# Performance work log

Measured on AMD Instinct MI355X. Metric: run time of the kernel, lower is better.

The kernel has to match this reference:

```python
import jax, jax.numpy as jnp
import numpy as np

B = 65536      # batch
HID = 128      # hidden_dim
Q = 4          # IRK stages
DT = 0.1       # default time step
N_ITERS = 10   # fixed-point iterations


def setup_inputs() -> dict:
    key = jax.random.key(0)
    ks = jax.random.split(key, 16)
    def lin(k, fan_in, fan_out):
        return jax.random.normal(k, (fan_in, fan_out), jnp.float32) / np.sqrt(fan_in)
    return {
        "X0": jax.random.normal(ks[0], (B, 4), jnp.float32),
        "W1": lin(ks[1], 4, HID),   "b1": jnp.zeros((HID,), jnp.float32),
        "W2": lin(ks[2], HID, HID), "b2": jnp.zeros((HID,), jnp.float32),
        "W3": lin(ks[3], HID, HID), "b3": jnp.zeros((HID,), jnp.float32),
        "W4": lin(ks[4], HID, 4),   "b4": jnp.zeros((4,), jnp.float32),
        "lam1": jax.random.normal(ks[5], (1,), jnp.float32) * 0.1 + 0.5,
        "lam2": jax.random.normal(ks[6], (1,), jnp.float32) * 0.1 + 0.5,
        "lam3": jax.random.normal(ks[7], (1,), jnp.float32) * 0.1 + 0.5,
        "lam4": jax.random.normal(ks[8], (1,), jnp.float32) * 0.1 + 0.5,
        "IRK_alpha": jax.random.normal(ks[9], (Q, Q), jnp.float32) * 0.25,
        "IRK_beta": jax.random.normal(ks[10], (Q,), jnp.float32) * 0.25,
    }


def reference(X0, W1, b1, W2, b2, W3, b3, W4, b4,
              lam1, lam2, lam3, lam4, IRK_alpha, IRK_beta):
    dt = DT

    def mlp(x):  # (N,4) -> (N,4)
        h = jnp.tanh(x @ W1 + b1)
        h = jnp.tanh(h @ W2 + b2)
        h = jnp.tanh(h @ W3 + b3)
        return h @ W4 + b4

    def hamiltonian_vf(x):  # x: (N,4) = [p1,p2,q1,q2]
        H_out = mlp(x)
        dp_dt = -lam1 * H_out[:, 2:] - lam2 * x[:, 2:]
        dq_dt = lam3 * H_out[:, :2] + lam4 * x[:, :2]
        return jnp.concatenate([dp_dt, dq_dt], axis=1)

    bsz = X0.shape[0]
    K = jnp.zeros((bsz, Q, 4), X0.dtype)
    for _ in range(N_ITERS):  # small fixed trip count, unrolled
        # same contraction as original torch einsum 'bqi,ij->bqj'
        X_stages = X0[:, None, :] + dt * jnp.einsum('bqi,ij->bqj', K, IRK_alpha)
        K = hamiltonian_vf(X_stages.reshape(-1, 4)).reshape(bsz, Q, 4)

    # intended IRK final combine: X1 = X0 + dt * sum_q beta_q K[:,q,:]
    X1 = X0 + dt * jnp.einsum('bqi,q->bi', K, IRK_beta)
    return X1
```

## Files before the change

kernel.cpp:

```cpp
#include <hip/hip_runtime.h>
#include <hip/hip_bf16.h>
#include <stdint.h>

#define HID    128
#define DT     0.1f
#define NITER  10
#define NTHR   512
#define NW     8
#define RPW    32
#define NBLK   256
#define NCH    4
#define SCALE  2.885390081777927f

typedef __attribute__((ext_vector_type(8))) short bf16x8;
typedef __attribute__((ext_vector_type(4))) float f32x4;
typedef __attribute__((ext_vector_type(2))) unsigned int u32x2;
typedef __attribute__((ext_vector_type(4))) unsigned int u32x4;

union FragU { bf16x8 v; uint32_t u[4]; };

struct alignas(16) Smem {
    uint32_t w2f[8 * 4 * 64 * 4];
    uint32_t w3f[8 * 4 * 64 * 4];
    uint32_t w1f[8 * 64 * 4];
    float    b1[HID], b2[HID], b3[HID];
    uint16_t hbuf[NW * RPW * HID];
};

__device__ __forceinline__ uint16_t f2bf(float f) {
    uint32_t u = __float_as_uint(f);
    return (uint16_t)((u + 0x7fffu + ((u >> 16) & 1u)) >> 16);
}

__device__ __forceinline__ uint32_t pk2(float a, float b) {
    __hip_bfloat162 h = __float22bfloat162_rn(float2{a, b});
    return *reinterpret_cast<uint32_t*>(&h);
}

__device__ __forceinline__ float tanh_pre(float y) {
    float e = __builtin_amdgcn_exp2f(y);
    return fmaf(-2.0f, __builtin_amdgcn_rcpf(e + 1.0f), 1.0f);
}

__device__ __forceinline__ float uread(const float* p) {
    return __uint_as_float(__builtin_amdgcn_readfirstlane(__float_as_uint(*p)));
}

__device__ __forceinline__ void hstore(char* hb, int row, int ot, int g, const f32x4& a) {
    int off = row * 256 + ((32 * ot + 8 * g) ^ ((row & 7) << 4));
    u32x2 p;
    p.x = pk2(tanh_pre(a[0]), tanh_pre(a[1]));
    p.y = pk2(tanh_pre(a[2]), tanh_pre(a[3]));
    *(u32x2*)(hb + off) = p;
}

__device__ __forceinline__ bf16x8 hload(const char* hb, int row, int kt, int g) {
    int off = row * 256 + ((64 * kt + 16 * g) ^ ((row & 7) << 4));
    return *(const bf16x8*)(hb + off);
}

__device__ __forceinline__ void dense_layer(
    char* hb, const uint32_t* __restrict__ wf, const float* __restrict__ bias,
    int ln, int g, int lane)
{
    bf16x8 hf[2][4];
    #pragma unroll
    for (int ct = 0; ct < 2; ++ct)
        #pragma unroll
        for (int kt = 0; kt < 4; ++kt)
            hf[ct][kt] = hload(hb, ct * 16 + ln, kt, g);
    #pragma unroll
    for (int ot = 0; ot < 8; ++ot) {
        f32x4 bs = *(const f32x4*)&bias[ot * 16 + 4 * g];
        f32x4 aA = bs, aB = bs;
        #pragma unroll
        for (int kt = 0; kt < 4; ++kt) {
            bf16x8 wfr = *(const bf16x8*)&wf[((ot * 4 + kt) * 64 + lane) * 4];
            aA = __builtin_amdgcn_mfma_f32_16x16x32_bf16(wfr, hf[0][kt], aA, 0, 0, 0);
            aB = __builtin_amdgcn_mfma_f32_16x16x32_bf16(wfr, hf[1][kt], aB, 0, 0, 0);
        }
        hstore(hb, ln, ot, g, aA);
        hstore(hb, 16 + ln, ot, g, aB);
    }
}

__global__ __launch_bounds__(NTHR, 2) void pinn_irk_rows(
    const float* __restrict__ x0g,
    const float* __restrict__ w1g, const float* __restrict__ b1g,
    const float* __restrict__ w2g, const float* __restrict__ b2g,
    const float* __restrict__ w3g, const float* __restrict__ b3g,
    const float* __restrict__ w4g, const float* __restrict__ b4g,
    const float* __restrict__ l1g, const float* __restrict__ l2g,
    const float* __restrict__ l3g, const float* __restrict__ l4g,
    const float* __restrict__ alg, const float* __restrict__ beg,
    float* __restrict__ outg)
{
    __shared__ Smem S;
    const int t    = threadIdx.x;
    const int blk  = blockIdx.x;
    const int lane = t & 63;
    const int w    = t >> 6;
    const int ln   = lane & 15;
    const int g    = lane >> 4;
    const bool owner = (g == 0);

    const float L0 = uread(l1g), L1v = uread(l2g), L2v = uread(l3g), L3v = uread(l4g);
    const float B40 = uread(b4g), B41 = uread(b4g + 1);
    const float B42 = uread(b4g + 2), B43 = uread(b4g + 3);
    const float BE0 = uread(beg), BE1 = uread(beg + 1);
    const float BE2 = uread(beg + 2), BE3 = uread(beg + 3);
    float A[16];
    #pragma unroll
    for (int i = 0; i < 16; ++i) A[i] = uread(alg + i);

    for (int s = t; s < 2048; s += NTHR) {
        int lane_s = s & 63, kto = s >> 6;
        int kt = kto & 3, ot = kto >> 2;
        int m = ot * 16 + (lane_s & 15), gs = lane_s >> 4;
        uint32_t f2[4], f3[4];
        #pragma unroll
        for (int jj = 0; jj < 4; ++jj) {
            int k = kt * 32 + 8 * gs + 2 * jj;
            f2[jj] = (uint32_t)f2bf(w2g[k * HID + m] * SCALE)
                   | ((uint32_t)f2bf(w2g[(k + 1) * HID + m] * SCALE) << 16);
            f3[jj] = (uint32_t)f2bf(w3g[k * HID + m] * SCALE)
                   | ((uint32_t)f2bf(w3g[(k + 1) * HID + m] * SCALE) << 16);
        }
        *(u32x4*)&S.w2f[s * 4] = (u32x4){f2[0], f2[1], f2[2], f2[3]};
        *(u32x4*)&S.w3f[s * 4] = (u32x4){f3[0], f3[1], f3[2], f3[3]};
    }
    {
        int lane_s = t & 63, ot = t >> 6;
        int gs = lane_s >> 4;
        uint32_t f[4] = {0u, 0u, 0u, 0u};
        if (gs == 0) {
            int m = ot * 16 + (lane_s & 15);
            f[0] = (uint32_t)f2bf(w1g[0 * HID + m] * SCALE)
                 | ((uint32_t)f2bf(w1g[1 * HID + m] * SCALE) << 16);
            f[1] = (uint32_t)f2bf(w1g[2 * HID + m] * SCALE)
                 | ((uint32_t)f2bf(w1g[3 * HID + m] * SCALE) << 16);
        }
        *(u32x4*)&S.w1f[t * 4] = (u32x4){f[0], f[1], f[2], f[3]};
    }
    if (t < HID) {
        S.b1[t] = b1g[t] * SCALE;
        S.b2[t] = b2g[t] * SCALE;
        S.b3[t] = b3g[t] * SCALE;
    }
    bf16x8 w4f[4];
    #pragma unroll
    for (int kt = 0; kt < 4; ++kt) {
        bf16x8 f;
        #pragma unroll
        for (int j = 0; j < 8; ++j) {
            int k = kt * 32 + 8 * g + j;
            f[j] = (ln < 4) ? (short)f2bf(w4g[k * 4 + ln]) : (short)0;
        }
        w4f[kt] = f;
    }
    __syncthreads();

    char* hb = (char*)&S.hbuf[w * RPW * HID];

    for (int ch = 0; ch < NCH; ++ch) {
        const int base = ((blk * NW + w) * NCH + ch) * RPW;
        f32x4 XA0 = *(const f32x4*)&x0g[((base + ln) >> 2) * 4];
        f32x4 XB0 = *(const f32x4*)&x0g[((base + 16 + ln) >> 2) * 4];
        f32x4 XA = XA0, XB = XB0;
        f32x4 kvA = {0.f,0.f,0.f,0.f}, kvB = {0.f,0.f,0.f,0.f};

        #pragma unroll 1
        for (int it = 0; it < NITER; ++it) {
            FragU xa, xb;
            xa.u[0] = owner ? pk2(XA[0], XA[1]) : 0u;
            xa.u[1] = owner ? pk2(XA[2], XA[3]) : 0u;
            xa.u[2] = 0u; xa.u[3] = 0u;
            xb.u[0] = owner ? pk2(XB[0], XB[1]) : 0u;
            xb.u[1] = owner ? pk2(XB[2], XB[3]) : 0u;
            xb.u[2] = 0u; xb.u[3] = 0u;

            #pragma unroll
            for (int ot = 0; ot < 8; ++ot) {
                f32x4 bs = *(const f32x4*)&S.b1[ot * 16 + 4 * g];
                bf16x8 wfr = *(const bf16x8*)&S.w1f[(ot * 64 + lane) * 4];
                f32x4 aA = __builtin_amdgcn_mfma_f32_16x16x32_bf16(wfr, xa.v, bs, 0, 0, 0);
                f32x4 aB = __builtin_amdgcn_mfma_f32_16x16x32_bf16(wfr, xb.v, bs, 0, 0, 0);
                hstore(hb, ln, ot, g, aA);
                hstore(hb, 16 + ln, ot, g, aB);
            }
            dense_layer(hb, S.w2f, S.b2, ln, g, lane);
            dense_layer(hb, S.w3f, S.b3, ln, g, lane);

            {
                bf16x8 hf[2][4];
                #pragma unroll
                for (int ct = 0; ct < 2; ++ct)
                    #pragma unroll
                    for (int kt = 0; kt < 4; ++kt)
                        hf[ct][kt] = hload(hb, ct * 16 + ln, kt, g);
                f32x4 kA = {0.f,0.f,0.f,0.f}, kB = {0.f,0.f,0.f,0.f};
                #pragma unroll
                for (int kt = 0; kt < 4; ++kt) {
                    kA = __builtin_amdgcn_mfma_f32_16x16x32_bf16(w4f[kt], hf[0][kt], kA, 0, 0, 0);
                    kB = __builtin_amdgcn_mfma_f32_16x16x32_bf16(w4f[kt], hf[1][kt], kB, 0, 0, 0);
                }
                float h0 = kA[0] + B40, h1 = kA[1] + B41;
                float h2 = kA[2] + B42, h3 = kA[3] + B43;
                kvA = (f32x4){-L0 * h2 - L1v * XA[2], -L0 * h3 - L1v * XA[3],
                               L2v * h0 + L3v * XA[0],  L2v * h1 + L3v * XA[1]};
                h0 = kB[0] + B40; h1 = kB[1] + B41;
                h2 = kB[2] + B42; h3 = kB[3] + B43;
                kvB = (f32x4){-L0 * h2 - L1v * XB[2], -L0 * h3 - L1v * XB[3],
                               L2v * h0 + L3v * XB[0],  L2v * h1 + L3v * XB[1]};
                #pragma unroll
                for (int c = 0; c < 4; ++c) {
                    float sA = kvA[0] * A[c] + kvA[1] * A[4 + c]
                             + kvA[2] * A[8 + c] + kvA[3] * A[12 + c];
                    float sB = kvB[0] * A[c] + kvB[1] * A[4 + c]
                             + kvB[2] * A[8 + c] + kvB[3] * A[12 + c];
                    XA[c] = fmaf(DT, sA, XA0[c]);
                    XB[c] = fmaf(DT, sB, XB0[c]);
                }
            }
        }

        if (owner) {
            *(f32x4*)(hb + ln * 16)        = kvA;
            *(f32x4*)(hb + (16 + ln) * 16) = kvB;
        }
        if (lane < 32) {
            const float* kk = (const float*)hb;
            int bl_ = lane >> 2, i = lane & 3;
            float s = BE0 * kk[(bl_ * 4 + 0) * 4 + i]
                    + BE1 * kk[(bl_ * 4 + 1) * 4 + i]
                    + BE2 * kk[(bl_ * 4 + 2) * 4 + i]
                    + BE3 * kk[(bl_ * 4 + 3) * 4 + i];
            int idx = base + lane;
            outg[idx] = x0g[idx] + DT * s;
        }
    }
}

extern "C" void kernel_launch(void* const* d_in, const int* in_sizes, int n_in,
                              void* d_out, int out_size, void* d_ws, size_t ws_size,
                              hipStream_t stream) {
    (void)in_sizes; (void)n_in; (void)d_ws; (void)ws_size; (void)out_size;

    dim3 grid(NBLK);
    dim3 block(NTHR);

    pinn_irk_rows<<<grid, block, 0, stream>>>(
        (const float*)d_in[0],
        (const float*)d_in[1],  (const float*)d_in[2],
        (const float*)d_in[3],  (const float*)d_in[4],
        (const float*)d_in[5],  (const float*)d_in[6],
        (const float*)d_in[7],  (const float*)d_in[8],
        (const float*)d_in[9],  (const float*)d_in[10],
        (const float*)d_in[11], (const float*)d_in[12],
        (const float*)d_in[13], (const float*)d_in[14],
        (float*)d_out);
}
```

Baseline: 405.6 us.

## Split rows across twice as many waves and batch tanh reciprocals

Doubles the block to 1024 threads (16 waves), so each wave handles 16 rows per chunk instead of 32 and issues one MFMA chain instead of two interleaved ones. This is meant to raise occupancy and latency hiding per CU. The cost is that each row now pulls twice as much weight-fragment traffic from LDS, and each wave has less instruction-level parallelism. The tanh is rewritten to compute four values with a single clamped reciprocal plus extra multiplies, cutting transcendental ops at some rounding risk. The launch bound asks for 4 blocks per CU, which may force tight register limits and cause spills.

```diff
diff --git a/kernel.cpp b/kernel.cpp
--- a/kernel.cpp
+++ b/kernel.cpp
@@ -5,9 +5,9 @@
 #define HID    128
 #define DT     0.1f
 #define NITER  10
-#define NTHR   512
-#define NW     8
-#define RPW    32
+#define NTHR   1024
+#define NW     16
+#define RPW    16
 #define NBLK   256
 #define NCH    4
 #define SCALE  2.885390081777927f
@@ -37,9 +37,23 @@
     return *reinterpret_cast<uint32_t*>(&h);
 }
 
-__device__ __forceinline__ float tanh_pre(float y) {
-    float e = __builtin_amdgcn_exp2f(y);
-    return fmaf(-2.0f, __builtin_amdgcn_rcpf(e + 1.0f), 1.0f);
+__device__ __forceinline__ f32x4 tanh4(f32x4 y) {
+    float e0 = __builtin_amdgcn_exp2f(fminf(y[0], 30.f)) + 1.0f;
+    float e1 = __builtin_amdgcn_exp2f(fminf(y[1], 30.f)) + 1.0f;
+    float e2 = __builtin_amdgcn_exp2f(fminf(y[2], 30.f)) + 1.0f;
+    float e3 = __builtin_amdgcn_exp2f(fminf(y[3], 30.f)) + 1.0f;
+    float p01   = e0 * e1;
+    float p012  = p01 * e2;
+    float p0123 = p012 * e3;
+    float r     = __builtin_amdgcn_rcpf(p0123);
+    float i3   = p012 * r;
+    float r012 = e3 * r;
+    float i2   = p01 * r012;
+    float r01  = e2 * r012;
+    float i1   = e0 * r01;
+    float i0   = e1 * r01;
+    return (f32x4){fmaf(-2.f, i0, 1.f), fmaf(-2.f, i1, 1.f),
+                   fmaf(-2.f, i2, 1.f), fmaf(-2.f, i3, 1.f)};
 }
 
 __device__ __forceinline__ float uread(const float* p) {
@@ -47,10 +61,11 @@
 }
 
 __device__ __forceinline__ void hstore(char* hb, int row, int ot, int g, const f32x4& a) {
+    f32x4 tq = tanh4(a);
     int off = row * 256 + ((32 * ot + 8 * g) ^ ((row & 7) << 4));
     u32x2 p;
-    p.x = pk2(tanh_pre(a[0]), tanh_pre(a[1]));
-    p.y = pk2(tanh_pre(a[2]), tanh_pre(a[3]));
+    p.x = pk2(tq[0], tq[1]);
+    p.y = pk2(tq[2], tq[3]);
     *(u32x2*)(hb + off) = p;
 }
 
@@ -63,28 +78,23 @@
     char* hb, const uint32_t* __restrict__ wf, const float* __restrict__ bias,
     int ln, int g, int lane)
 {
-    bf16x8 hf[2][4];
-    #pragma unroll
-    for (int ct = 0; ct < 2; ++ct)
-        #pragma unroll
-        for (int kt = 0; kt < 4; ++kt)
-            hf[ct][kt] = hload(hb, ct * 16 + ln, kt, g);
+    bf16x8 hf[4];
+    #pragma unroll
+    for (int kt = 0; kt < 4; ++kt)
+        hf[kt] = hload(hb, ln, kt, g);
     #pragma unroll
     for (int ot = 0; ot < 8; ++ot) {
-        f32x4 bs = *(const f32x4*)&bias[ot * 16 + 4 * g];
-        f32x4 aA = bs, aB = bs;
+        f32x4 a = *(const f32x4*)&bias[ot * 16 + 4 * g];
         #pragma unroll
         for (int kt = 0; kt < 4; ++kt) {
             bf16x8 wfr = *(const bf16x8*)&wf[((ot * 4 + kt) * 64 + lane) * 4];
-            aA = __builtin_amdgcn_mfma_f32_16x16x32_bf16(wfr, hf[0][kt], aA, 0, 0, 0);
-            aB = __builtin_amdgcn_mfma_f32_16x16x32_bf16(wfr, hf[1][kt], aB, 0, 0, 0);
-        }
-        hstore(hb, ln, ot, g, aA);
-        hstore(hb, 16 + ln, ot, g, aB);
-    }
-}
-
-__global__ __launch_bounds__(NTHR, 2) void pinn_irk_rows(
+            a = __builtin_amdgcn_mfma_f32_16x16x32_bf16(wfr, hf[kt], a, 0, 0, 0);
+        }
+        hstore(hb, ln, ot, g, a);
+    }
+}
+
+__global__ __launch_bounds__(NTHR, 4) void pinn_irk_rows(
     const float* __restrict__ x0g,
     const float* __restrict__ w1g, const float* __restrict__ b1g,
     const float* __restrict__ w2g, const float* __restrict__ b2g,
@@ -129,7 +139,7 @@
         *(u32x4*)&S.w2f[s * 4] = (u32x4){f2[0], f2[1], f2[2], f2[3]};
         *(u32x4*)&S.w3f[s * 4] = (u32x4){f3[0], f3[1], f3[2], f3[3]};
     }
-    {
+    if (t < 512) {
         int lane_s = t & 63, ot = t >> 6;
         int gs = lane_s >> 4;
         uint32_t f[4] = {0u, 0u, 0u, 0u};
@@ -165,70 +175,52 @@
     for (int ch = 0; ch < NCH; ++ch) {
         const int base = ((blk * NW + w) * NCH + ch) * RPW;
         f32x4 XA0 = *(const f32x4*)&x0g[((base + ln) >> 2) * 4];
-        f32x4 XB0 = *(const f32x4*)&x0g[((base + 16 + ln) >> 2) * 4];
-        f32x4 XA = XA0, XB = XB0;
-        f32x4 kvA = {0.f,0.f,0.f,0.f}, kvB = {0.f,0.f,0.f,0.f};
+        f32x4 XA = XA0;
+        f32x4 kvA = {0.f, 0.f, 0.f, 0.f};
 
         #pragma unroll 1
         for (int it = 0; it < NITER; ++it) {
-            FragU xa, xb;
+            FragU xa;
             xa.u[0] = owner ? pk2(XA[0], XA[1]) : 0u;
             xa.u[1] = owner ? pk2(XA[2], XA[3]) : 0u;
             xa.u[2] = 0u; xa.u[3] = 0u;
-            xb.u[0] = owner ? pk2(XB[0], XB[1]) : 0u;
-            xb.u[1] = owner ? pk2(XB[2], XB[3]) : 0u;
-            xb.u[2] = 0u; xb.u[3] = 0u;
 
             #pragma unroll
             for (int ot = 0; ot < 8; ++ot) {
                 f32x4 bs = *(const f32x4*)&S.b1[ot * 16 + 4 * g];
                 bf16x8 wfr = *(const bf16x8*)&S.w1f[(ot * 64 + lane) * 4];
-                f32x4 aA = __builtin_amdgcn_mfma_f32_16x16x32_bf16(wfr, xa.v, bs, 0, 0, 0);
-                f32x4 aB = __builtin_amdgcn_mfma_f32_16x16x32_bf16(wfr, xb.v, bs, 0, 0, 0);
-                hstore(hb, ln, ot, g, aA);
-                hstore(hb, 16 + ln, ot, g, aB);
+                f32x4 a = __builtin_amdgcn_mfma_f32_16x16x32_bf16(wfr, xa.v, bs, 0, 0, 0);
+                hstore(hb, ln, ot, g, a);
             }
             dense_layer(hb, S.w2f, S.b2, ln, g, lane);
             dense_layer(hb, S.w3f, S.b3, ln, g, lane);
 
             {
-                bf16x8 hf[2][4];
+                bf16x8 hf[4];
                 #pragma unroll
-                for (int ct = 0; ct < 2; ++ct)
-                    #pragma unroll
-                    for (int kt = 0; kt < 4; ++kt)
-                        hf[ct][kt] = hload(hb, ct * 16 + ln, kt, g);
-                f32x4 kA = {0.f,0.f,0.f,0.f}, kB = {0.f,0.f,0.f,0.f};
+                for (int kt = 0; kt < 4; ++kt)
+                    hf[kt] = hload(hb, ln, kt, g);
+                f32x4 kA = {0.f, 0.f, 0.f, 0.f};
                 #pragma unroll
-                for (int kt = 0; kt < 4; ++kt) {
-                    kA = __builtin_amdgcn_mfma_f32_16x16x32_bf16(w4f[kt], hf[0][kt], kA, 0, 0, 0);
-                    kB = __builtin_amdgcn_mfma_f32_16x16x32_bf16(w4f[kt], hf[1][kt], kB, 0, 0, 0);
-                }
+                for (int kt = 0; kt < 4; ++kt)
+                    kA = __builtin_amdgcn_mfma_f32_16x16x32_bf16(w4f[kt], hf[kt], kA, 0, 0, 0);
                 float h0 = kA[0] + B40, h1 = kA[1] + B41;
                 float h2 = kA[2] + B42, h3 = kA[3] + B43;
                 kvA = (f32x4){-L0 * h2 - L1v * XA[2], -L0 * h3 - L1v * XA[3],
                                L2v * h0 + L3v * XA[0],  L2v * h1 + L3v * XA[1]};
-                h0 = kB[0] + B40; h1 = kB[1] + B41;
-                h2 = kB[2] + B42; h3 = kB[3] + B43;
-                kvB = (f32x4){-L0 * h2 - L1v * XB[2], -L0 * h3 - L1v * XB[3],
-                               L2v * h0 + L3v * XB[0],  L2v * h1 + L3v * XB[1]};
                 #pragma unroll
                 for (int c = 0; c < 4; ++c) {
-                    float sA = kvA[0] * A[c] + kvA[1] * A[4 + c]
-                             + kvA[2] * A[8 + c] + kvA[3] * A[12 + c];
-                    float sB = kvB[0] * A[c] + kvB[1] * A[4 + c]
-                             + kvB[2] * A[8 + c] + kvB[3] * A[12 + c];
-                    XA[c] = fmaf(DT, sA, XA0[c]);
-                    XB[c] = fmaf(DT, sB, XB0[c]);
+                    float s = kvA[0] * A[c] + kvA[1] * A[4 + c]
+                            + kvA[2] * A[8 + c] + kvA[3] * A[12 + c];
+                    XA[c] = fmaf(DT, s, XA0[c]);
                 }
             }
         }
 
         if (owner) {
-            *(f32x4*)(hb + ln * 16)        = kvA;
-            *(f32x4*)(hb + (16 + ln) * 16) = kvB;
-        }
-        if (lane < 32) {
+            *(f32x4*)(hb + ln * 16) = kvA;
+        }
+        if (lane < 16) {
             const float* kk = (const float*)hb;
             int bl_ = lane >> 2, i = lane & 3;
             float s = BE0 * kk[(bl_ * 4 + 0) * 4 + i]
```

Result: slower. 474.8 us (+17.1%).

## Keep MLP activations in registers by permuting K ordering instead of LDS round-trips

Applied to the files above, without the earlier changes.

Each layer's MFMA output is now packed directly into the next layer's B-operand fragments in registers. The K index ordering of W1..W4 is permuted so the accumulator layout matches the fragment layout, which removes the per-layer LDS store and reload of the hidden activations. The LDS hidden buffer shrinks to a small K scratch area. The grid doubles and chunks per wave halve, and s_setprio is raised around the MFMA bursts. The cost is more live registers for the eight accumulator tiles per row group, which could pressure occupancy under the two-blocks-per-CU bound.

```diff
diff --git a/kernel.cpp b/kernel.cpp
--- a/kernel.cpp
+++ b/kernel.cpp
@@ -7,14 +7,12 @@
 #define NITER  10
 #define NTHR   512
 #define NW     8
-#define RPW    32
-#define NBLK   256
-#define NCH    4
+#define NBLK   512
+#define NCH    2
 #define SCALE  2.885390081777927f
 
 typedef __attribute__((ext_vector_type(8))) short bf16x8;
 typedef __attribute__((ext_vector_type(4))) float f32x4;
-typedef __attribute__((ext_vector_type(2))) unsigned int u32x2;
 typedef __attribute__((ext_vector_type(4))) unsigned int u32x4;
 
 union FragU { bf16x8 v; uint32_t u[4]; };
@@ -24,7 +22,7 @@
     uint32_t w3f[8 * 4 * 64 * 4];
     uint32_t w1f[8 * 64 * 4];
     float    b1[HID], b2[HID], b3[HID];
-    uint16_t hbuf[NW * RPW * HID];
+    float    kk[NW * 32 * 4];
 };
 
 __device__ __forceinline__ uint16_t f2bf(float f) {
@@ -46,45 +44,43 @@
     return __uint_as_float(__builtin_amdgcn_readfirstlane(__float_as_uint(*p)));
 }
 
-__device__ __forceinline__ void hstore(char* hb, int row, int ot, int g, const f32x4& a) {
-    int off = row * 256 + ((32 * ot + 8 * g) ^ ((row & 7) << 4));
-    u32x2 p;
-    p.x = pk2(tanh_pre(a[0]), tanh_pre(a[1]));
-    p.y = pk2(tanh_pre(a[2]), tanh_pre(a[3]));
-    *(u32x2*)(hb + off) = p;
-}
-
-__device__ __forceinline__ bf16x8 hload(const char* hb, int row, int kt, int g) {
-    int off = row * 256 + ((64 * kt + 16 * g) ^ ((row & 7) << 4));
-    return *(const bf16x8*)(hb + off);
-}
-
-__device__ __forceinline__ void dense_layer(
-    char* hb, const uint32_t* __restrict__ wf, const float* __restrict__ bias,
-    int ln, int g, int lane)
+__device__ __forceinline__ void packfr(const f32x4 (&a)[8], bf16x8 (&bfr)[4]) {
+    #pragma unroll
+    for (int kt = 0; kt < 4; ++kt) {
+        FragU f;
+        f.u[0] = pk2(tanh_pre(a[2 * kt][0]),     tanh_pre(a[2 * kt][1]));
+        f.u[1] = pk2(tanh_pre(a[2 * kt][2]),     tanh_pre(a[2 * kt][3]));
+        f.u[2] = pk2(tanh_pre(a[2 * kt + 1][0]), tanh_pre(a[2 * kt + 1][1]));
+        f.u[3] = pk2(tanh_pre(a[2 * kt + 1][2]), tanh_pre(a[2 * kt + 1][3]));
+        bfr[kt] = f.v;
+    }
+}
+
+__device__ __forceinline__ void dense_reg(
+    const uint32_t* __restrict__ wf, const float* __restrict__ bias,
+    bf16x8 (&bfrA)[4], bf16x8 (&bfrB)[4], int lane, int g)
 {
-    bf16x8 hf[2][4];
-    #pragma unroll
-    for (int ct = 0; ct < 2; ++ct)
-        #pragma unroll
-        for (int kt = 0; kt < 4; ++kt)
-            hf[ct][kt] = hload(hb, ct * 16 + ln, kt, g);
+    f32x4 aA[8], aB[8];
     #pragma unroll
     for (int ot = 0; ot < 8; ++ot) {
         f32x4 bs = *(const f32x4*)&bias[ot * 16 + 4 * g];
-        f32x4 aA = bs, aB = bs;
+        aA[ot] = bs; aB[ot] = bs;
+    }
+    __builtin_amdgcn_s_setprio(1);
+    #pragma unroll
+    for (int ot = 0; ot < 8; ++ot)
         #pragma unroll
         for (int kt = 0; kt < 4; ++kt) {
             bf16x8 wfr = *(const bf16x8*)&wf[((ot * 4 + kt) * 64 + lane) * 4];
-            aA = __builtin_amdgcn_mfma_f32_16x16x32_bf16(wfr, hf[0][kt], aA, 0, 0, 0);
-            aB = __builtin_amdgcn_mfma_f32_16x16x32_bf16(wfr, hf[1][kt], aB, 0, 0, 0);
-        }
-        hstore(hb, ln, ot, g, aA);
-        hstore(hb, 16 + ln, ot, g, aB);
-    }
-}
-
-__global__ __launch_bounds__(NTHR, 2) void pinn_irk_rows(
+            aA[ot] = __builtin_amdgcn_mfma_f32_16x16x32_bf16(wfr, bfrA[kt], aA[ot], 0, 0, 0);
+            aB[ot] = __builtin_amdgcn_mfma_f32_16x16x32_bf16(wfr, bfrB[kt], aB[ot], 0, 0, 0);
+        }
+    __builtin_amdgcn_s_setprio(0);
+    packfr(aA, bfrA);
+    packfr(aB, bfrB);
+}
+
+__global__ __launch_bounds__(NTHR, 2) void pinn_irk_reg(
     const float* __restrict__ x0g,
     const float* __restrict__ w1g, const float* __restrict__ b1g,
     const float* __restrict__ w2g, const float* __restrict__ b2g,
@@ -120,7 +116,7 @@
         uint32_t f2[4], f3[4];
         #pragma unroll
         for (int jj = 0; jj < 4; ++jj) {
-            int k = kt * 32 + 8 * gs + 2 * jj;
+            int k = 16 * (2 * kt + (jj >> 1)) + 4 * gs + 2 * (jj & 1);
             f2[jj] = (uint32_t)f2bf(w2g[k * HID + m] * SCALE)
                    | ((uint32_t)f2bf(w2g[(k + 1) * HID + m] * SCALE) << 16);
             f3[jj] = (uint32_t)f2bf(w3g[k * HID + m] * SCALE)
@@ -129,7 +125,7 @@
         *(u32x4*)&S.w2f[s * 4] = (u32x4){f2[0], f2[1], f2[2], f2[3]};
         *(u32x4*)&S.w3f[s * 4] = (u32x4){f3[0], f3[1], f3[2], f3[3]};
     }
-    {
+    if (t < 512) {
         int lane_s = t & 63, ot = t >> 6;
         int gs = lane_s >> 4;
         uint32_t f[4] = {0u, 0u, 0u, 0u};
@@ -153,21 +149,19 @@
         bf16x8 f;
         #pragma unroll
         for (int j = 0; j < 8; ++j) {
-            int k = kt * 32 + 8 * g + j;
+            int k = 16 * (2 * kt + (j >> 2)) + 4 * g + (j & 3);
             f[j] = (ln < 4) ? (short)f2bf(w4g[k * 4 + ln]) : (short)0;
         }
         w4f[kt] = f;
     }
     __syncthreads();
 
-    char* hb = (char*)&S.hbuf[w * RPW * HID];
-
     for (int ch = 0; ch < NCH; ++ch) {
-        const int base = ((blk * NW + w) * NCH + ch) * RPW;
+        const int base = ((blk * NW + w) * NCH + ch) * 32;
         f32x4 XA0 = *(const f32x4*)&x0g[((base + ln) >> 2) * 4];
         f32x4 XB0 = *(const f32x4*)&x0g[((base + 16 + ln) >> 2) * 4];
         f32x4 XA = XA0, XB = XB0;
-        f32x4 kvA = {0.f,0.f,0.f,0.f}, kvB = {0.f,0.f,0.f,0.f};
+        f32x4 kvA = {0.f, 0.f, 0.f, 0.f}, kvB = {0.f, 0.f, 0.f, 0.f};
 
         #pragma unroll 1
         for (int it = 0; it < NITER; ++it) {
@@ -179,31 +173,32 @@
             xb.u[1] = owner ? pk2(XB[2], XB[3]) : 0u;
             xb.u[2] = 0u; xb.u[3] = 0u;
 
+            f32x4 aA[8], aB[8];
+            __builtin_amdgcn_s_setprio(1);
             #pragma unroll
             for (int ot = 0; ot < 8; ++ot) {
                 f32x4 bs = *(const f32x4*)&S.b1[ot * 16 + 4 * g];
                 bf16x8 wfr = *(const bf16x8*)&S.w1f[(ot * 64 + lane) * 4];
-                f32x4 aA = __builtin_amdgcn_mfma_f32_16x16x32_bf16(wfr, xa.v, bs, 0, 0, 0);
-                f32x4 aB = __builtin_amdgcn_mfma_f32_16x16x32_bf16(wfr, xb.v, bs, 0, 0, 0);
-                hstore(hb, ln, ot, g, aA);
-                hstore(hb, 16 + ln, ot, g, aB);
+                aA[ot] = __builtin_amdgcn_mfma_f32_16x16x32_bf16(wfr, xa.v, bs, 0, 0, 0);
+                aB[ot] = __builtin_amdgcn_mfma_f32_16x16x32_bf16(wfr, xb.v, bs, 0, 0, 0);
             }
-            dense_layer(hb, S.w2f, S.b2, ln, g, lane);
-            dense_layer(hb, S.w3f, S.b3, ln, g, lane);
-
+            __builtin_amdgcn_s_setprio(0);
+            bf16x8 bfrA[4], bfrB[4];
+            packfr(aA, bfrA);
+            packfr(aB, bfrB);
+
+            dense_reg(S.w2f, S.b2, bfrA, bfrB, lane, g);
+            dense_reg(S.w3f, S.b3, bfrA, bfrB, lane, g);
+
+            f32x4 kA = {0.f, 0.f, 0.f, 0.f}, kB = {0.f, 0.f, 0.f, 0.f};
+            __builtin_amdgcn_s_setprio(1);
+            #pragma unroll
+            for (int kt = 0; kt < 4; ++kt) {
+                kA = __builtin_amdgcn_mfma_f32_16x16x32_bf16(w4f[kt], bfrA[kt], kA, 0, 0, 0);
+                kB = __builtin_amdgcn_mfma_f32_16x16x32_bf16(w4f[kt], bfrB[kt], kB, 0, 0, 0);
+            }
+            __builtin_amdgcn_s_setprio(0);
             {
-                bf16x8 hf[2][4];
-                #pragma unroll
-                for (int ct = 0; ct < 2; ++ct)
-                    #pragma unroll
-                    for (int kt = 0; kt < 4; ++kt)
-                        hf[ct][kt] = hload(hb, ct * 16 + ln, kt, g);
-                f32x4 kA = {0.f,0.f,0.f,0.f}, kB = {0.f,0.f,0.f,0.f};
-                #pragma unroll
-                for (int kt = 0; kt < 4; ++kt) {
-                    kA = __builtin_amdgcn_mfma_f32_16x16x32_bf16(w4f[kt], hf[0][kt], kA, 0, 0, 0);
-                    kB = __builtin_amdgcn_mfma_f32_16x16x32_bf16(w4f[kt], hf[1][kt], kB, 0, 0, 0);
-                }
                 float h0 = kA[0] + B40, h1 = kA[1] + B41;
                 float h2 = kA[2] + B42, h3 = kA[3] + B43;
                 kvA = (f32x4){-L0 * h2 - L1v * XA[2], -L0 * h3 - L1v * XA[3],
@@ -224,17 +219,17 @@
             }
         }
 
+        float* kkw = &S.kk[w * 128];
         if (owner) {
-            *(f32x4*)(hb + ln * 16)        = kvA;
-            *(f32x4*)(hb + (16 + ln) * 16) = kvB;
+            *(f32x4*)&kkw[ln * 4]        = kvA;
+            *(f32x4*)&kkw[(16 + ln) * 4] = kvB;
         }
         if (lane < 32) {
-            const float* kk = (const float*)hb;
             int bl_ = lane >> 2, i = lane & 3;
-            float s = BE0 * kk[(bl_ * 4 + 0) * 4 + i]
-                    + BE1 * kk[(bl_ * 4 + 1) * 4 + i]
-                    + BE2 * kk[(bl_ * 4 + 2) * 4 + i]
-                    + BE3 * kk[(bl_ * 4 + 3) * 4 + i];
+            float s = BE0 * kkw[(bl_ * 4 + 0) * 4 + i]
+                    + BE1 * kkw[(bl_ * 4 + 1) * 4 + i]
+                    + BE2 * kkw[(bl_ * 4 + 2) * 4 + i]
+                    + BE3 * kkw[(bl_ * 4 + 3) * 4 + i];
             int idx = base + lane;
             outg[idx] = x0g[idx] + DT * s;
         }
@@ -249,7 +244,7 @@
     dim3 grid(NBLK);
     dim3 block(NTHR);
 
-    pinn_irk_rows<<<grid, block, 0, stream>>>(
+    pinn_irk_reg<<<grid, block, 0, stream>>>(
         (const float*)d_in[0],
         (const float*)d_in[1],  (const float*)d_in[2],
         (const float*)d_in[3],  (const float*)d_in[4],
```

Result: slower. 1.188 ms (+192.8%).
